# Kernel tuning notes

Measured on AMD Instinct MI355X. Metric: run time of the kernel, lower is better.

## Reference

```python
import jax, jax.numpy as jnp
import numpy as np

BITS = 4
N_LEVELS = 2 ** BITS
MINQ, MAXQ = 0, N_LEVELS - 1  # asymmetric (sym=False)
EPS = 1e-8
NORM = 2.4  # lp_loss exponent used inside find_params


def _find_params(x, num):
    """MSE grid search for per-channel scale/zero of a 2D weight x: [C, N].
    Faithful to Quantizer.find_params(x, weight=True) with mse=True, sym=False.
    """
    C = x.shape[0]
    zero_c = jnp.zeros((C,), x.dtype)
    xmin = jnp.minimum(x.min(axis=1), zero_c)
    xmax = jnp.maximum(x.max(axis=1), zero_c)
    xrange = xmax - xmin  # tmp_min is zeros, so range == xmax - xmin
    zps = jnp.arange(N_LEVELS, dtype=x.dtype)  # [Z] zero-point candidates
    cols = jnp.arange(C)

    def step(carry, i):
        best_score, best_min, best_max = carry
        tmp_max = xrange / num * i                       # [C]
        scale = jnp.maximum(tmp_max / (MAXQ - MINQ), EPS)  # [C] (tmp_min == 0)
        delta = scale
        x_round = jnp.round(x / scale[:, None])          # [C, N]
        # vectorize the inner zero-point loop over Z candidates
        new_min = -zps[:, None] * delta[None, :]         # [Z, C]
        new_max = tmp_max[None, :] - zps[:, None] * delta[None, :]  # [Z, C]
        zero = jnp.clip(MINQ - jnp.round(new_min / delta[None, :]), MINQ, MAXQ)  # [Z, C]
        q = jnp.clip(x_round[None, :, :] + zero[:, :, None], MINQ, MAXQ)  # [Z, C, N]
        x_q = scale[None, :, None] * (q - zero[:, :, None])               # [Z, C, N]
        score = jnp.mean(jnp.abs(x[None, :, :] - x_q) ** NORM, axis=2)    # [Z, C]
        # sequential 'score < best' keeps first minimum on ties -> argmin matches
        zbest = jnp.argmin(score, axis=0)                # [C]
        s = score[zbest, cols]
        nm = new_min[zbest, cols]
        nx = new_max[zbest, cols]
        upd = s < best_score
        best_min = jnp.where(upd, nm, best_min)
        best_max = jnp.where(upd, nx, best_max)
        best_score = jnp.minimum(best_score, s)
        return (best_score, best_min, best_max), None

    init = (jnp.full((C,), 1e10, x.dtype), xmin, xmax)
    iters = jnp.arange(1, num + 1, dtype=x.dtype)
    (_, best_min, best_max), _ = jax.lax.scan(jax.checkpoint(step), init, iters)

    min_val_neg = jnp.minimum(best_min, 0.0)
    max_val_pos = jnp.maximum(best_max, 0.0)
    scale = jnp.maximum((max_val_pos - min_val_neg) / (MAXQ - MINQ), EPS)
    zero = jnp.clip(MINQ - jnp.round(min_val_neg / scale), MINQ, MAXQ)
    # weight=True -> reshape to [-1, 1] for broadcasting over fan-in
    return scale[:, None], zero[:, None]


def reference(x, num):
    scale, zero = _find_params(x, num)
    q = jnp.clip(jnp.round(x / scale) + zero, MINQ, MAXQ)
    return scale * (q - zero)


def setup_inputs() -> dict:
    key = jax.random.key(0)
    x = jax.random.normal(key, (1024, 4096), dtype=jnp.float32)
    return {"x": x, "num": 100}
```

## Files before the change

kernel.cpp:

```cpp
#include <hip/hip_runtime.h>

#define NE 4096
#define BLK 512
#define NWAVE (BLK / 64)

__device__ __forceinline__ float pow24(float d) {
    float d2 = d * d;
    return __builtin_amdgcn_exp2f(1.2f * __builtin_amdgcn_logf(d2));
}

__global__ __launch_bounds__(BLK) void quant_kernel(const float* __restrict__ x,
                                                    float* __restrict__ out,
                                                    const int* __restrict__ nump) {
    const int c = blockIdx.x;
    const int tid = threadIdx.x;
    const int lane = tid & 63;
    const int wv = tid >> 6;
    const int num = *nump;

    __shared__ float sx[NE];
    __shared__ float fsc[NWAVE], ffi[NWAVE], fmn[NWAVE], fmx[NWAVE];

    const float* xrow = x + (size_t)c * NE;
    for (int idx = tid; idx < NE; idx += BLK) sx[idx] = xrow[idx];
    __syncthreads();

    for (int k = 2; k <= NE; k <<= 1) {
        for (int j = k >> 1; j > 0; j >>= 1) {
            for (int base = tid; base < NE; base += BLK) {
                int ixj = base ^ j;
                if (ixj > base) {
                    float a = sx[base], b = sx[ixj];
                    if (((base & k) == 0) ? (a > b) : (a < b)) { sx[base] = b; sx[ixj] = a; }
                }
            }
            __syncthreads();
        }
    }

    const float xmn = fminf(sx[0], 0.0f);
    const float xmx = fmaxf(sx[NE - 1], 0.0f);
    const float xrange = xmx - xmn;
    const float rdn = xrange / (float)num;

    const int zmy = ((lane & 1) << 3) | ((lane & 2) << 1) | ((lane & 4) >> 1) | ((lane & 8) >> 3);
    const float zmyf = (float)zmy;

    float best_score = 1e10f;
    float best_fi = 1e9f;
    float best_min = xmn, best_max = xmx;

    for (int i = wv + 1; i <= num; i += NWAVE) {
        const float fi = (float)i;
        const float tmp_max = rdn * fi;
        const float s = fmaxf(tmp_max / 15.0f, 1e-8f);
        const float ns = -s;
        const float rs = 1.0f / s;

        float tacc = 0.0f;
        float corr[16];
#pragma unroll
        for (int z = 0; z < 16; ++z) corr[z] = 0.0f;

        for (int cc = 0; cc < 64; ++cc) {
            const float xe = sx[(cc << 6) + lane];
            const float r = rintf(xe * rs);
            const float p_in = pow24(fmaf(ns, r, xe));
            tacc += p_in;

            const float rmaxw = __int_as_float(__builtin_amdgcn_readlane(__float_as_int(r), 63));
            const float rminw = __int_as_float(__builtin_amdgcn_readlane(__float_as_int(r), 0));
            const int nhi = (int)fminf(fmaxf(rmaxw, 0.0f), 16.0f);
            const int nlo = (int)fminf(fmaxf(-rminw, 0.0f), 16.0f);

#pragma unroll
            for (int j = 0; j < 16; ++j) {
                if (j >= nhi) break;
                const float jf = (float)j;
                const float ph = pow24(fmaf(ns, jf, xe));
                corr[15 - j] += (r > jf) ? (ph - p_in) : 0.0f;
            }
#pragma unroll
            for (int j = 0; j < 16; ++j) {
                if (j >= nlo) break;
                const float jf = (float)j;
                const float pl = pow24(fmaf(s, jf, xe));
                corr[j] += (r < -jf) ? (pl - p_in) : 0.0f;
            }
        }

#pragma unroll
        for (int k = 1; k < 64; k <<= 1) tacc += __shfl_xor(tacc, k, 64);

#pragma unroll
        for (int q = 0; q < 8; ++q) {
            float send = (lane & 1) ? corr[q] : corr[q + 8];
            float keep = (lane & 1) ? corr[q + 8] : corr[q];
            corr[q] = keep + __shfl_xor(send, 1, 64);
        }
#pragma unroll
        for (int q = 0; q < 4; ++q) {
            float send = (lane & 2) ? corr[q] : corr[q + 4];
            float keep = (lane & 2) ? corr[q + 4] : corr[q];
            corr[q] = keep + __shfl_xor(send, 2, 64);
        }
#pragma unroll
        for (int q = 0; q < 2; ++q) {
            float send = (lane & 4) ? corr[q] : corr[q + 2];
            float keep = (lane & 4) ? corr[q + 2] : corr[q];
            corr[q] = keep + __shfl_xor(send, 4, 64);
        }
        {
            float send = (lane & 8) ? corr[0] : corr[1];
            float keep = (lane & 8) ? corr[1] : corr[0];
            corr[0] = keep + __shfl_xor(send, 8, 64);
        }
        corr[0] += __shfl_xor(corr[0], 16, 64);
        corr[0] += __shfl_xor(corr[0], 32, 64);
        float sc = (tacc + corr[0]) * (1.0f / 4096.0f);

        float bsz = sc, bzz = zmyf;
#pragma unroll
        for (int k = 1; k < 64; k <<= 1) {
            float os = __shfl_xor(bsz, k, 64);
            float oz = __shfl_xor(bzz, k, 64);
            bool take = (os < bsz) || ((os == bsz) && (oz < bzz));
            bsz = take ? os : bsz;
            bzz = take ? oz : bzz;
        }
        if (bsz < best_score) {
            best_score = bsz;
            best_fi = fi;
            float zs = bzz * s;
            best_min = -zs;
            best_max = tmp_max - zs;
        }
    }

    if (lane == 0) { fsc[wv] = best_score; ffi[wv] = best_fi; fmn[wv] = best_min; fmx[wv] = best_max; }
    __syncthreads();
    float bs = fsc[0], bi = ffi[0], bm = fmn[0], bxv = fmx[0];
#pragma unroll
    for (int w = 1; w < NWAVE; ++w) {
        bool take = (fsc[w] < bs) || ((fsc[w] == bs) && (ffi[w] < bi));
        if (take) { bs = fsc[w]; bi = ffi[w]; bm = fmn[w]; bxv = fmx[w]; }
    }

    const float min_neg = fminf(bm, 0.0f);
    const float max_pos = fmaxf(bxv, 0.0f);
    const float scale = fmaxf((max_pos - min_neg) / 15.0f, 1e-8f);
    const float zero = fminf(fmaxf(0.0f - rintf(min_neg / scale), 0.0f), 15.0f);

    float* orow = out + (size_t)c * NE;
    for (int idx = tid; idx < NE; idx += BLK) {
        float xe = xrow[idx];
        float q = fminf(fmaxf(rintf(xe / scale) + zero, 0.0f), 15.0f);
        orow[idx] = scale * (q - zero);
    }
}

extern "C" void kernel_launch(void* const* d_in, const int* in_sizes, int n_in,
                              void* d_out, int out_size, void* d_ws, size_t ws_size,
                              hipStream_t stream) {
    const float* x = (const float*)d_in[0];
    const int* nump = (const int*)d_in[1];
    float* out = (float*)d_out;
    const int C = out_size / NE;
    quant_kernel<<<C, BLK, 0, stream>>>(x, out, nump);
}
```

Before: 1.161 ms.

## Split sorted chunks into fully-saturated and mixed ranges for the score loop

Binary-searches the sorted row to find the leading and trailing 64-element chunks whose rounded values are all saturated (r <= -16 or r >= 16). For those chunks it accumulates all 16 zero-point errors directly with no rounding, readlane or branch logic, and runs the original correction loop only on the middle chunks. Inside the mixed loop the conditional select is replaced by an fminf/fmaxf clamp on the argument, and the loop bounds are made wave-uniform with readfirstlane. The saturated chunks still do 16 pow evaluations each, so the saving depends on how many chunks saturate.

```diff
diff --git a/kernel.cpp b/kernel.cpp
--- a/kernel.cpp
+++ b/kernel.cpp
@@ -54,38 +54,71 @@
         const float fi = (float)i;
         const float tmp_max = rdn * fi;
         const float s = fmaxf(tmp_max / 15.0f, 1e-8f);
-        const float ns = -s;
         const float rs = 1.0f / s;
+
+        float smU[16];
+#pragma unroll
+        for (int j = 0; j < 16; ++j) smU[j] = s * (float)j;
+
+        int A = 0;
+#pragma unroll
+        for (int st = 64; st >= 1; st >>= 1) {
+            int cand = A + st;
+            if (cand <= 64) {
+                float rv = rintf(sx[((cand - 1) << 6) + 63] * rs);
+                if (rv <= -16.0f) A = cand;
+            }
+        }
+        int B = 0;
+#pragma unroll
+        for (int st = 64; st >= 1; st >>= 1) {
+            int cand = B + st;
+            if (cand <= 64) {
+                float rv = rintf(sx[((cand - 1) << 6)] * rs);
+                if (rv < 16.0f) B = cand;
+            }
+        }
 
         float tacc = 0.0f;
         float corr[16];
 #pragma unroll
         for (int z = 0; z < 16; ++z) corr[z] = 0.0f;
 
-        for (int cc = 0; cc < 64; ++cc) {
+        for (int cc = 0; cc < A; ++cc) {
+            const float xe = sx[(cc << 6) + lane];
+#pragma unroll
+            for (int j = 0; j < 16; ++j) corr[j] += pow24(xe + smU[j]);
+        }
+        for (int cc = B; cc < 64; ++cc) {
+            const float xe = sx[(cc << 6) + lane];
+#pragma unroll
+            for (int j = 0; j < 16; ++j) corr[15 - j] += pow24(xe - smU[j]);
+        }
+        for (int cc = A; cc < B; ++cc) {
             const float xe = sx[(cc << 6) + lane];
             const float r = rintf(xe * rs);
-            const float p_in = pow24(fmaf(ns, r, xe));
+            const float sr = s * r;
+            const float p_in = pow24(xe - sr);
             tacc += p_in;
 
-            const float rmaxw = __int_as_float(__builtin_amdgcn_readlane(__float_as_int(r), 63));
-            const float rminw = __int_as_float(__builtin_amdgcn_readlane(__float_as_int(r), 0));
-            const int nhi = (int)fminf(fmaxf(rmaxw, 0.0f), 16.0f);
-            const int nlo = (int)fminf(fmaxf(-rminw, 0.0f), 16.0f);
+            int rmaxi = (int)__int_as_float(__builtin_amdgcn_readlane(__float_as_int(r), 63));
+            int rmini = (int)__int_as_float(__builtin_amdgcn_readlane(__float_as_int(r), 0));
+            int nhi = rmaxi < 0 ? 0 : (rmaxi > 16 ? 16 : rmaxi);
+            int nlo = rmini > 0 ? 0 : (-rmini > 16 ? 16 : -rmini);
+            nhi = __builtin_amdgcn_readfirstlane(nhi);
+            nlo = __builtin_amdgcn_readfirstlane(nlo);
 
 #pragma unroll
             for (int j = 0; j < 16; ++j) {
                 if (j >= nhi) break;
-                const float jf = (float)j;
-                const float ph = pow24(fmaf(ns, jf, xe));
-                corr[15 - j] += (r > jf) ? (ph - p_in) : 0.0f;
+                const float arg = xe - fminf(sr, smU[j]);
+                corr[15 - j] += pow24(arg) - p_in;
             }
 #pragma unroll
             for (int j = 0; j < 16; ++j) {
                 if (j >= nlo) break;
-                const float jf = (float)j;
-                const float pl = pow24(fmaf(s, jf, xe));
-                corr[j] += (r < -jf) ? (pl - p_in) : 0.0f;
+                const float arg = xe - fmaxf(sr, -smU[j]);
+                corr[j] += pow24(arg) - p_in;
             }
         }
 
```

New measurement: 1.263 ms. +8.8%, slower.
